# Performance work log

Hardware: AMD Instinct MI355X
Metric: run time of the kernel (lower is better)

The kernel has to match this reference:

```python
import jax, jax.numpy as jnp
import numpy as np

NUM_NODES = 2048   # N (spatial)
SEQ_LEN = 512      # T (temporal)
LATENT = 32
LAYERS = 2
SELF_LOOP_EPS = 0.5
B = 4


def setup_inputs() -> dict:
    key = jax.random.key(0)
    k1, k2, k3 = jax.random.split(key, 3)
    NT = NUM_NODES + SEQ_LEN
    X = jax.random.normal(k1, (B, NT, LATENT), dtype=jnp.float32)
    # GraphSAGE-style per-layer weights: self and neighbor transforms + bias
    Ws = jax.random.normal(k2, (LAYERS, LATENT, LATENT), dtype=jnp.float32) * 0.05
    Wn = jax.random.normal(k3, (LAYERS, LATENT, LATENT), dtype=jnp.float32) * 0.05
    b = jnp.zeros((LAYERS, LATENT), dtype=jnp.float32)
    return {"X": X, "Ws": Ws, "Wn": Wn, "b": b}


def build_adj(X):
    # node_embs = concat(spatial, temporal) == X itself
    adj = jnp.einsum('bnf,bmf->bnm', X, X)          # [B, N+T, N+T]
    adj = jnp.tanh(jax.nn.relu(adj))
    NT = X.shape[1]
    adj = adj + SELF_LOOP_EPS * jnp.eye(NT, dtype=adj.dtype)
    return adj


def reference(X, Ws, Wn, b):
    adj = build_adj(X)
    h = X
    # dense weighted aggregation == sparse message passing over nonzero edges,
    # since edge weights are exactly the adjacency values
    for l in range(LAYERS):
        agg = jnp.einsum('bnm,bmd->bnd', adj, h)    # neighbor aggregation
        h = jax.nn.elu(jnp.einsum('bnd,de->bne', h, Ws[l])
                       + jnp.einsum('bnd,de->bne', agg, Wn[l])
                       + b[l])
    return h
```

## Files before the change

### kernel.cpp

```cpp
#include <hip/hip_runtime.h>
#include <math.h>

#define NT 2560
#define DF 32
#define NB 4
#define SELF_EPS 0.5f
#define MS 8
#define MROWS (NT / MS)
#define MT 64
#define MITERS (MROWS / MT)
#define TN 64

typedef __attribute__((ext_vector_type(8))) short bf16x8;
typedef __attribute__((ext_vector_type(4))) float f32x4;

__device__ __forceinline__ unsigned short f2bf(float f) {
    unsigned u = __builtin_bit_cast(unsigned, f);
    u += 0x7fffu + ((u >> 16) & 1u);
    return (unsigned short)(u >> 16);
}

__device__ __forceinline__ float fast_rcp(float x) {
#if __has_builtin(__builtin_amdgcn_rcpf)
    return __builtin_amdgcn_rcpf(x);
#else
    return 1.0f / x;
#endif
}

__device__ __forceinline__ float fast_exp2(float x) {
#if __has_builtin(__builtin_amdgcn_exp2f)
    return __builtin_amdgcn_exp2f(x);
#else
    return exp2f(x);
#endif
}

__device__ __forceinline__ float tanh_relu(float x) {
    float m = fmaxf(x, 0.0f);
    float e = fast_exp2(m * 2.885390082f);
    return 1.0f - 2.0f * fast_rcp(e + 1.0f);
}

__global__ __launch_bounds__(256, 4)
void prep(const float* __restrict__ X,
          unsigned short* __restrict__ Xb, unsigned short* __restrict__ XT)
{
    const int t = threadIdx.x;
    __shared__ float sT[32][33];
    const int tile = blockIdx.x;
    const int b = tile / 80, n0 = (tile % 80) * 32;
    const int row = t >> 3, c4 = (t & 7) * 4;
    const size_t rbase = ((size_t)(b * NT + n0 + row)) * DF + c4;
    const float4 v = *(const float4*)(X + rbase);
    unsigned p0 = (unsigned)f2bf(v.x) | ((unsigned)f2bf(v.y) << 16);
    unsigned p1 = (unsigned)f2bf(v.z) | ((unsigned)f2bf(v.w) << 16);
    *(uint2*)(Xb + rbase) = make_uint2(p0, p1);
    sT[row][c4 + 0] = v.x; sT[row][c4 + 1] = v.y;
    sT[row][c4 + 2] = v.z; sT[row][c4 + 3] = v.w;
    __syncthreads();
    const int d = t >> 3, nq = (t & 7) * 4;
    unsigned q0 = (unsigned)f2bf(sT[nq + 0][d]) | ((unsigned)f2bf(sT[nq + 1][d]) << 16);
    unsigned q1 = (unsigned)f2bf(sT[nq + 2][d]) | ((unsigned)f2bf(sT[nq + 3][d]) << 16);
    *(uint2*)(XT + ((size_t)(b * DF + d)) * NT + n0 + nq) = make_uint2(q0, q1);
}

__global__ __launch_bounds__(256, 4)
void gsage_main(const unsigned short* __restrict__ Xb,
                const unsigned short* __restrict__ HT,
                float* __restrict__ part)
{
    __shared__ unsigned short XmL[64 * 40];
    __shared__ unsigned short HtL[32 * 72];
    __shared__ unsigned short Ss[4 * 16 * 72];

    const int t = threadIdx.x;
    const int w = t >> 6, lane = t & 63;
    const int q = lane >> 4, c = lane & 15;
    const int n0 = blockIdx.x * TN;
    const int slice = blockIdx.y;
    const int mbase = slice * MROWS;
    const int b = blockIdx.z;

    const size_t xbase = (size_t)b * NT * DF;
    const size_t tbase = (size_t)b * DF * NT;

    const bf16x8 bfn = *(const bf16x8*)(Xb + xbase + (size_t)(n0 + w * 16 + c) * DF + q * 8);

    f32x4 acc0 = {0.f, 0.f, 0.f, 0.f};
    f32x4 acc1 = {0.f, 0.f, 0.f, 0.f};

    const int xrow = t >> 2, xseg = t & 3;
    const int hrow = t >> 3, hseg = t & 7;

    uint4 xv = *(const uint4*)(Xb + xbase + (size_t)(mbase + xrow) * DF + xseg * 8);
    uint4 hv = *(const uint4*)(HT + tbase + (size_t)hrow * NT + mbase + hseg * 8);

    const int n_g = n0 + w * 16 + c;
    unsigned short* SsW = Ss + w * (16 * 72);

    for (int it = 0; it < MITERS; ++it) {
        const int m0 = mbase + it * MT;
        __syncthreads();
        *(uint4*)(XmL + xrow * 40 + xseg * 8) = xv;
        *(uint4*)(HtL + hrow * 72 + hseg * 8) = hv;
        if (it + 1 < MITERS) {
            const int m1 = m0 + MT;
            xv = *(const uint4*)(Xb + xbase + (size_t)(m1 + xrow) * DF + xseg * 8);
            hv = *(const uint4*)(HT + tbase + (size_t)hrow * NT + m1 + hseg * 8);
        }
        __syncthreads();

        #pragma unroll
        for (int t4 = 0; t4 < 4; ++t4) {
            const bf16x8 af = *(const bf16x8*)(XmL + (t4 * 16 + c) * 40 + q * 8);
            const f32x4 zero = {0.f, 0.f, 0.f, 0.f};
            f32x4 st = __builtin_amdgcn_mfma_f32_16x16x32_bf16(af, bfn, zero, 0, 0, 0);
            float v0 = tanh_relu(st[0]);
            float v1 = tanh_relu(st[1]);
            float v2 = tanh_relu(st[2]);
            float v3 = tanh_relu(st[3]);
            if ((n0 + w * 16 == m0 + t4 * 16) && (q == (c >> 2))) {
                const int r = c & 3;
                v0 += (r == 0) ? SELF_EPS : 0.f;
                v1 += (r == 1) ? SELF_EPS : 0.f;
                v2 += (r == 2) ? SELF_EPS : 0.f;
                v3 += (r == 3) ? SELF_EPS : 0.f;
            }
            unsigned p0 = (unsigned)f2bf(v0) | ((unsigned)f2bf(v1) << 16);
            unsigned p1 = (unsigned)f2bf(v2) | ((unsigned)f2bf(v3) << 16);
            *(uint2*)(SsW + c * 72 + t4 * 16 + q * 4) = make_uint2(p0, p1);
        }
        asm volatile("s_waitcnt lgkmcnt(0)" ::: "memory");

        #pragma unroll
        for (int kc = 0; kc < 2; ++kc) {
            const bf16x8 sf = *(const bf16x8*)(SsW + c * 72 + kc * 32 + q * 8);
            const bf16x8 h0 = *(const bf16x8*)(HtL + c * 72 + kc * 32 + q * 8);
            const bf16x8 h1 = *(const bf16x8*)(HtL + (16 + c) * 72 + kc * 32 + q * 8);
            acc0 = __builtin_amdgcn_mfma_f32_16x16x32_bf16(sf, h0, acc0, 0, 0, 0);
            acc1 = __builtin_amdgcn_mfma_f32_16x16x32_bf16(sf, h1, acc1, 0, 0, 0);
        }
    }

    float* pp = part + ((size_t)slice * NB) * NT * DF + xbase
                     + (size_t)(n0 + w * 16 + q * 4) * DF + c;
    #pragma unroll
    for (int r = 0; r < 4; ++r) {
        pp[(size_t)r * DF]      = acc0[r];
        pp[(size_t)r * DF + 16] = acc1[r];
    }
}

__global__ __launch_bounds__(256, 4)
void gsage_epi(const float* __restrict__ Hin, const float* __restrict__ part,
               const float* __restrict__ Wsl, const float* __restrict__ Wnl,
               const float* __restrict__ bl,
               float* __restrict__ Hout, unsigned short* __restrict__ HTout)
{
    __shared__ float sW[32][33], sN[32][33], sH[32][36], sA[32][36], sT[32][33];
    const int t = threadIdx.x;
    const int n0 = blockIdx.x * 32;
    const int b = blockIdx.y;
    const int row = t >> 3, c4 = (t & 7) * 4;
    const size_t rb = ((size_t)(b * NT + n0 + row)) * DF + c4;
    const float4 hv = *(const float4*)(Hin + rb);
    float4 av = make_float4(0.f, 0.f, 0.f, 0.f);
    #pragma unroll
    for (int s = 0; s < MS; ++s) {
        const float4 v = *(const float4*)(part + (size_t)s * NB * NT * DF + rb);
        av.x += v.x; av.y += v.y; av.z += v.z; av.w += v.w;
    }
    const float4 w0 = *(const float4*)(Wsl + row * DF + c4);
    const float4 w1 = *(const float4*)(Wnl + row * DF + c4);
    sH[row][c4+0]=hv.x; sH[row][c4+1]=hv.y; sH[row][c4+2]=hv.z; sH[row][c4+3]=hv.w;
    sA[row][c4+0]=av.x; sA[row][c4+1]=av.y; sA[row][c4+2]=av.z; sA[row][c4+3]=av.w;
    sW[row][c4+0]=w0.x; sW[row][c4+1]=w0.y; sW[row][c4+2]=w0.z; sW[row][c4+3]=w0.w;
    sN[row][c4+0]=w1.x; sN[row][c4+1]=w1.y; sN[row][c4+2]=w1.z; sN[row][c4+3]=w1.w;
    __syncthreads();

    float4 z = make_float4(bl[c4+0], bl[c4+1], bl[c4+2], bl[c4+3]);
    #pragma unroll
    for (int k = 0; k < DF; ++k) {
        const float hk = sH[row][k], ak = sA[row][k];
        z.x += hk * sW[k][c4+0] + ak * sN[k][c4+0];
        z.y += hk * sW[k][c4+1] + ak * sN[k][c4+1];
        z.z += hk * sW[k][c4+2] + ak * sN[k][c4+2];
        z.w += hk * sW[k][c4+3] + ak * sN[k][c4+3];
    }
    z.x = z.x > 0.f ? z.x : __expf(z.x) - 1.f;
    z.y = z.y > 0.f ? z.y : __expf(z.y) - 1.f;
    z.z = z.z > 0.f ? z.z : __expf(z.z) - 1.f;
    z.w = z.w > 0.f ? z.w : __expf(z.w) - 1.f;
    *(float4*)(Hout + rb) = z;

    if (HTout != nullptr) {
        sT[row][c4+0]=z.x; sT[row][c4+1]=z.y; sT[row][c4+2]=z.z; sT[row][c4+3]=z.w;
        __syncthreads();
        const int d = t >> 3, nq = (t & 7) * 4;
        unsigned q0 = (unsigned)f2bf(sT[nq+0][d]) | ((unsigned)f2bf(sT[nq+1][d]) << 16);
        unsigned q1 = (unsigned)f2bf(sT[nq+2][d]) | ((unsigned)f2bf(sT[nq+3][d]) << 16);
        *(uint2*)(HTout + ((size_t)(b * DF + d)) * NT + n0 + nq) = make_uint2(q0, q1);
    }
}

extern "C" void kernel_launch(void* const* d_in, const int* in_sizes, int n_in,
                              void* d_out, int out_size, void* d_ws, size_t ws_size,
                              hipStream_t stream) {
    const float* X  = (const float*)d_in[0];
    const float* Ws = (const float*)d_in[1];
    const float* Wn = (const float*)d_in[2];
    const float* bv = (const float*)d_in[3];
    float* out = (float*)d_out;

    char* ws = (char*)d_ws;
    float* part = (float*)ws;
    float* h1   = part + (size_t)MS * NB * NT * DF;
    unsigned short* Xb  = (unsigned short*)(ws + 11796480);
    unsigned short* XT  = Xb + (size_t)NB * NT * DF;
    unsigned short* H1T = XT + (size_t)NB * NT * DF;

    prep<<<320, 256, 0, stream>>>(X, Xb, XT);

    dim3 g(NT / TN, MS, NB);
    gsage_main<<<g, 256, 0, stream>>>(Xb, XT, part);
    gsage_epi<<<dim3(NT / 32, NB), 256, 0, stream>>>(X, part, Ws, Wn, bv, h1, H1T);
    gsage_main<<<g, 256, 0, stream>>>(Xb, H1T, part);
    gsage_epi<<<dim3(NT / 32, NB), 256, 0, stream>>>(h1, part, Ws + DF * DF, Wn + DF * DF,
                                                     bv + DF, out, nullptr);
}
```

Measured before the change: 106.1 us.

## Fuse prep and both layers into one cooperative kernel with grid sync

Replaces the five-launch pipeline (prep, two main passes with split-M partials, two epilogues) with a single cooperative kernel that uses grid.sync between stages. Each 128-thread block owns 16 output rows, and its two waves each cover half of the M range with per-wave LDS staging. The partial sums are reduced in shared memory and the epilogue runs in-block, which removes the partial-sum buffer traffic and the separate epilogue launches. The cost is far fewer rows per block, no cross-wave reuse of the X and H tiles, and grid-wide barriers, with a fallback to three separate launches if the cooperative launch fails.

Measured after the change: 409.3 us. +285.9%, slower.

```diff
diff --git a/kernel.cpp b/kernel.cpp
--- a/kernel.cpp
+++ b/kernel.cpp
@@ -1,15 +1,15 @@
 #include <hip/hip_runtime.h>
+#include <hip/hip_cooperative_groups.h>
 #include <math.h>
+
+namespace cg = cooperative_groups;
 
 #define NT 2560
 #define DF 32
 #define NB 4
 #define SELF_EPS 0.5f
-#define MS 8
-#define MROWS (NT / MS)
-#define MT 64
-#define MITERS (MROWS / MT)
-#define TN 64
+#define WREG 12032
+#define MITW 20
 
 typedef __attribute__((ext_vector_type(8))) short bf16x8;
 typedef __attribute__((ext_vector_type(4))) float f32x4;
@@ -19,7 +19,6 @@
     u += 0x7fffu + ((u >> 16) & 1u);
     return (unsigned short)(u >> 16);
 }
-
 __device__ __forceinline__ float fast_rcp(float x) {
 #if __has_builtin(__builtin_amdgcn_rcpf)
     return __builtin_amdgcn_rcpf(x);
@@ -27,7 +26,6 @@
     return 1.0f / x;
 #endif
 }
-
 __device__ __forceinline__ float fast_exp2(float x) {
 #if __has_builtin(__builtin_amdgcn_exp2f)
     return __builtin_amdgcn_exp2f(x);
@@ -35,92 +33,108 @@
     return exp2f(x);
 #endif
 }
-
 __device__ __forceinline__ float tanh_relu(float x) {
     float m = fmaxf(x, 0.0f);
     float e = fast_exp2(m * 2.885390082f);
     return 1.0f - 2.0f * fast_rcp(e + 1.0f);
 }
-
-__global__ __launch_bounds__(256, 4)
-void prep(const float* __restrict__ X,
-          unsigned short* __restrict__ Xb, unsigned short* __restrict__ XT)
-{
-    const int t = threadIdx.x;
-    __shared__ float sT[32][33];
-    const int tile = blockIdx.x;
-    const int b = tile / 80, n0 = (tile % 80) * 32;
+__device__ __forceinline__ float elu(float x) {
+    return x > 0.f ? x : fast_exp2(x * 1.442695041f) - 1.f;
+}
+
+
+__device__ __forceinline__ void prep_unit(const float* __restrict__ X,
+                                          unsigned short* __restrict__ Xb,
+                                          unsigned short* __restrict__ XT,
+                                          char* smem, int t, int blk)
+{
+    const int b = blk & 3, n0p = (blk >> 2) * 16;
+    float* sTp = (float*)smem;
     const int row = t >> 3, c4 = (t & 7) * 4;
-    const size_t rbase = ((size_t)(b * NT + n0 + row)) * DF + c4;
-    const float4 v = *(const float4*)(X + rbase);
+    const size_t off = ((size_t)b * NT + n0p + row) * DF + c4;
+    const float4 v = *(const float4*)(X + off);
     unsigned p0 = (unsigned)f2bf(v.x) | ((unsigned)f2bf(v.y) << 16);
     unsigned p1 = (unsigned)f2bf(v.z) | ((unsigned)f2bf(v.w) << 16);
-    *(uint2*)(Xb + rbase) = make_uint2(p0, p1);
-    sT[row][c4 + 0] = v.x; sT[row][c4 + 1] = v.y;
-    sT[row][c4 + 2] = v.z; sT[row][c4 + 3] = v.w;
+    *(uint2*)(Xb + off) = make_uint2(p0, p1);
+    sTp[row * 33 + c4 + 0] = v.x; sTp[row * 33 + c4 + 1] = v.y;
+    sTp[row * 33 + c4 + 2] = v.z; sTp[row * 33 + c4 + 3] = v.w;
     __syncthreads();
-    const int d = t >> 3, nq = (t & 7) * 4;
-    unsigned q0 = (unsigned)f2bf(sT[nq + 0][d]) | ((unsigned)f2bf(sT[nq + 1][d]) << 16);
-    unsigned q1 = (unsigned)f2bf(sT[nq + 2][d]) | ((unsigned)f2bf(sT[nq + 3][d]) << 16);
-    *(uint2*)(XT + ((size_t)(b * DF + d)) * NT + n0 + nq) = make_uint2(q0, q1);
-}
-
-__global__ __launch_bounds__(256, 4)
-void gsage_main(const unsigned short* __restrict__ Xb,
-                const unsigned short* __restrict__ HT,
-                float* __restrict__ part)
-{
-    __shared__ unsigned short XmL[64 * 40];
-    __shared__ unsigned short HtL[32 * 72];
-    __shared__ unsigned short Ss[4 * 16 * 72];
-
-    const int t = threadIdx.x;
+    const int d = t >> 2, mp = (t & 3) * 4;
+    unsigned q0 = (unsigned)f2bf(sTp[(mp + 0) * 33 + d])
+                | ((unsigned)f2bf(sTp[(mp + 1) * 33 + d]) << 16);
+    unsigned q1 = (unsigned)f2bf(sTp[(mp + 2) * 33 + d])
+                | ((unsigned)f2bf(sTp[(mp + 3) * 33 + d]) << 16);
+    *(uint2*)(XT + ((size_t)b * DF + d) * NT + n0p + mp) = make_uint2(q0, q1);
+}
+
+__device__ __forceinline__ void layer_pass(
+    const unsigned short* __restrict__ Xb,
+    const unsigned short* __restrict__ HT,
+    const float* __restrict__ Hin,
+    const float* __restrict__ Wsl, const float* __restrict__ Wnl,
+    const float* __restrict__ bl,
+    float* __restrict__ Hout,
+    unsigned short* __restrict__ HTout,
+    char* smem, int t, int blk)
+{
+    const int b  = blk & 3;
+    const int n0 = (blk >> 2) * 16;
     const int w = t >> 6, lane = t & 63;
     const int q = lane >> 4, c = lane & 15;
-    const int n0 = blockIdx.x * TN;
-    const int slice = blockIdx.y;
-    const int mbase = slice * MROWS;
-    const int b = blockIdx.z;
-
     const size_t xbase = (size_t)b * NT * DF;
     const size_t tbase = (size_t)b * DF * NT;
 
-    const bf16x8 bfn = *(const bf16x8*)(Xb + xbase + (size_t)(n0 + w * 16 + c) * DF + q * 8);
+    unsigned short* Sw = (unsigned short*)(smem + w * WREG);
+    unsigned short* Xw = (unsigned short*)(smem + w * WREG + 2304);
+    unsigned short* Hw = (unsigned short*)(smem + w * WREG + 7424);
+
+    const bf16x8 bfn = *(const bf16x8*)(Xb + xbase + (size_t)(n0 + c) * DF + q * 8);
 
     f32x4 acc0 = {0.f, 0.f, 0.f, 0.f};
     f32x4 acc1 = {0.f, 0.f, 0.f, 0.f};
-
-    const int xrow = t >> 2, xseg = t & 3;
-    const int hrow = t >> 3, hseg = t & 7;
-
-    uint4 xv = *(const uint4*)(Xb + xbase + (size_t)(mbase + xrow) * DF + xseg * 8);
-    uint4 hv = *(const uint4*)(HT + tbase + (size_t)hrow * NT + mbase + hseg * 8);
-
-    const int n_g = n0 + w * 16 + c;
-    unsigned short* SsW = Ss + w * (16 * 72);
-
-    for (int it = 0; it < MITERS; ++it) {
-        const int m0 = mbase + it * MT;
-        __syncthreads();
-        *(uint4*)(XmL + xrow * 40 + xseg * 8) = xv;
-        *(uint4*)(HtL + hrow * 72 + hseg * 8) = hv;
-        if (it + 1 < MITERS) {
-            const int m1 = m0 + MT;
-            xv = *(const uint4*)(Xb + xbase + (size_t)(m1 + xrow) * DF + xseg * 8);
-            hv = *(const uint4*)(HT + tbase + (size_t)hrow * NT + m1 + hseg * 8);
-        }
-        __syncthreads();
+    const int wbase = w * (NT / 2);
+    const int hd = lane & 31, hh = lane >> 5;
+
+    uint4 xv[4], hv[4];
+    {
+        const unsigned short* xs = Xb + xbase + (size_t)(wbase + lane) * DF;
+        const unsigned short* hs = HT + tbase + (size_t)hd * NT + wbase + hh * 32;
+        #pragma unroll
+        for (int k = 0; k < 4; ++k) {
+            xv[k] = *(const uint4*)(xs + k * 8);
+            hv[k] = *(const uint4*)(hs + k * 8);
+        }
+    }
+
+    for (int it = 0; it < MITW; ++it) {
+        const int m0 = wbase + it * 64;
+        #pragma unroll
+        for (int k = 0; k < 4; ++k) {
+            *(uint4*)(Xw + lane * 40 + k * 8) = xv[k];
+            *(uint4*)(Hw + hd * 72 + hh * 32 + k * 8) = hv[k];
+        }
+        if (it + 1 < MITW) {
+            const int m1 = m0 + 64;
+            const unsigned short* xs = Xb + xbase + (size_t)(m1 + lane) * DF;
+            const unsigned short* hs = HT + tbase + (size_t)hd * NT + m1 + hh * 32;
+            #pragma unroll
+            for (int k = 0; k < 4; ++k) {
+                xv[k] = *(const uint4*)(xs + k * 8);
+                hv[k] = *(const uint4*)(hs + k * 8);
+            }
+        }
+        asm volatile("s_waitcnt lgkmcnt(0)" ::: "memory");
 
         #pragma unroll
         for (int t4 = 0; t4 < 4; ++t4) {
-            const bf16x8 af = *(const bf16x8*)(XmL + (t4 * 16 + c) * 40 + q * 8);
+            const bf16x8 af = *(const bf16x8*)(Xw + (t4 * 16 + c) * 40 + q * 8);
             const f32x4 zero = {0.f, 0.f, 0.f, 0.f};
             f32x4 st = __builtin_amdgcn_mfma_f32_16x16x32_bf16(af, bfn, zero, 0, 0, 0);
             float v0 = tanh_relu(st[0]);
             float v1 = tanh_relu(st[1]);
             float v2 = tanh_relu(st[2]);
             float v3 = tanh_relu(st[3]);
-            if ((n0 + w * 16 == m0 + t4 * 16) && (q == (c >> 2))) {
+            if ((m0 + t4 * 16 == n0) && (q == (c >> 2))) {
                 const int r = c & 3;
                 v0 += (r == 0) ? SELF_EPS : 0.f;
                 v1 += (r == 1) ? SELF_EPS : 0.f;
@@ -129,79 +143,125 @@
             }
             unsigned p0 = (unsigned)f2bf(v0) | ((unsigned)f2bf(v1) << 16);
             unsigned p1 = (unsigned)f2bf(v2) | ((unsigned)f2bf(v3) << 16);
-            *(uint2*)(SsW + c * 72 + t4 * 16 + q * 4) = make_uint2(p0, p1);
+            *(uint2*)(Sw + c * 72 + t4 * 16 + q * 4) = make_uint2(p0, p1);
         }
         asm volatile("s_waitcnt lgkmcnt(0)" ::: "memory");
 
         #pragma unroll
         for (int kc = 0; kc < 2; ++kc) {
-            const bf16x8 sf = *(const bf16x8*)(SsW + c * 72 + kc * 32 + q * 8);
-            const bf16x8 h0 = *(const bf16x8*)(HtL + c * 72 + kc * 32 + q * 8);
-            const bf16x8 h1 = *(const bf16x8*)(HtL + (16 + c) * 72 + kc * 32 + q * 8);
+            const bf16x8 sf  = *(const bf16x8*)(Sw + c * 72 + kc * 32 + q * 8);
+            const bf16x8 h0  = *(const bf16x8*)(Hw + c * 72 + kc * 32 + q * 8);
+            const bf16x8 h1v = *(const bf16x8*)(Hw + (16 + c) * 72 + kc * 32 + q * 8);
             acc0 = __builtin_amdgcn_mfma_f32_16x16x32_bf16(sf, h0, acc0, 0, 0, 0);
-            acc1 = __builtin_amdgcn_mfma_f32_16x16x32_bf16(sf, h1, acc1, 0, 0, 0);
-        }
-    }
-
-    float* pp = part + ((size_t)slice * NB) * NT * DF + xbase
-                     + (size_t)(n0 + w * 16 + q * 4) * DF + c;
+            acc1 = __builtin_amdgcn_mfma_f32_16x16x32_bf16(sf, h1v, acc1, 0, 0, 0);
+        }
+    }
+
+    float* sF = (float*)(smem + w * WREG);
     #pragma unroll
     for (int r = 0; r < 4; ++r) {
-        pp[(size_t)r * DF]      = acc0[r];
-        pp[(size_t)r * DF + 16] = acc1[r];
-    }
-}
-
-__global__ __launch_bounds__(256, 4)
-void gsage_epi(const float* __restrict__ Hin, const float* __restrict__ part,
-               const float* __restrict__ Wsl, const float* __restrict__ Wnl,
-               const float* __restrict__ bl,
-               float* __restrict__ Hout, unsigned short* __restrict__ HTout)
-{
-    __shared__ float sW[32][33], sN[32][33], sH[32][36], sA[32][36], sT[32][33];
-    const int t = threadIdx.x;
-    const int n0 = blockIdx.x * 32;
-    const int b = blockIdx.y;
-    const int row = t >> 3, c4 = (t & 7) * 4;
-    const size_t rb = ((size_t)(b * NT + n0 + row)) * DF + c4;
-    const float4 hv = *(const float4*)(Hin + rb);
-    float4 av = make_float4(0.f, 0.f, 0.f, 0.f);
-    #pragma unroll
-    for (int s = 0; s < MS; ++s) {
-        const float4 v = *(const float4*)(part + (size_t)s * NB * NT * DF + rb);
-        av.x += v.x; av.y += v.y; av.z += v.z; av.w += v.w;
-    }
-    const float4 w0 = *(const float4*)(Wsl + row * DF + c4);
-    const float4 w1 = *(const float4*)(Wnl + row * DF + c4);
-    sH[row][c4+0]=hv.x; sH[row][c4+1]=hv.y; sH[row][c4+2]=hv.z; sH[row][c4+3]=hv.w;
-    sA[row][c4+0]=av.x; sA[row][c4+1]=av.y; sA[row][c4+2]=av.z; sA[row][c4+3]=av.w;
-    sW[row][c4+0]=w0.x; sW[row][c4+1]=w0.y; sW[row][c4+2]=w0.z; sW[row][c4+3]=w0.w;
-    sN[row][c4+0]=w1.x; sN[row][c4+1]=w1.y; sN[row][c4+2]=w1.z; sN[row][c4+3]=w1.w;
+        sF[(q * 4 + r) * 33 + c]      = acc0[r];
+        sF[(q * 4 + r) * 33 + c + 16] = acc1[r];
+    }
     __syncthreads();
 
-    float4 z = make_float4(bl[c4+0], bl[c4+1], bl[c4+2], bl[c4+3]);
+    float* sAgg = (float*)(smem + 2304);
+    float* sOut = (float*)(smem + 2304 + 2112);
+    float* sH   = (float*)(smem + 7424);
+    float* sW   = (float*)(smem + WREG + 2304);
+    float* sN   = (float*)(smem + WREG + 7424);
+
+    const int rn = t >> 3, c4 = (t & 7) * 4;
+    {
+        const float* f0 = (const float*)(smem);
+        const float* f1 = (const float*)(smem + WREG);
+        #pragma unroll
+        for (int j = 0; j < 4; ++j)
+            sAgg[rn * 33 + c4 + j] = f0[rn * 33 + c4 + j] + f1[rn * 33 + c4 + j];
+        const float4 hvv = *(const float4*)(Hin + ((size_t)b * NT + n0 + rn) * DF + c4);
+        sH[rn * 33 + c4 + 0] = hvv.x; sH[rn * 33 + c4 + 1] = hvv.y;
+        sH[rn * 33 + c4 + 2] = hvv.z; sH[rn * 33 + c4 + 3] = hvv.w;
+        #pragma unroll
+        for (int h = 0; h < 2; ++h) {
+            const int k = rn + h * 16;
+            const float4 w0 = *(const float4*)(Wsl + k * DF + c4);
+            const float4 w1 = *(const float4*)(Wnl + k * DF + c4);
+            sW[k * 33 + c4 + 0] = w0.x; sW[k * 33 + c4 + 1] = w0.y;
+            sW[k * 33 + c4 + 2] = w0.z; sW[k * 33 + c4 + 3] = w0.w;
+            sN[k * 33 + c4 + 0] = w1.x; sN[k * 33 + c4 + 1] = w1.y;
+            sN[k * 33 + c4 + 2] = w1.z; sN[k * 33 + c4 + 3] = w1.w;
+        }
+    }
+    __syncthreads();
+
+    float z0 = bl[c4 + 0], z1 = bl[c4 + 1], z2 = bl[c4 + 2], z3 = bl[c4 + 3];
     #pragma unroll
     for (int k = 0; k < DF; ++k) {
-        const float hk = sH[row][k], ak = sA[row][k];
-        z.x += hk * sW[k][c4+0] + ak * sN[k][c4+0];
-        z.y += hk * sW[k][c4+1] + ak * sN[k][c4+1];
-        z.z += hk * sW[k][c4+2] + ak * sN[k][c4+2];
-        z.w += hk * sW[k][c4+3] + ak * sN[k][c4+3];
-    }
-    z.x = z.x > 0.f ? z.x : __expf(z.x) - 1.f;
-    z.y = z.y > 0.f ? z.y : __expf(z.y) - 1.f;
-    z.z = z.z > 0.f ? z.z : __expf(z.z) - 1.f;
-    z.w = z.w > 0.f ? z.w : __expf(z.w) - 1.f;
-    *(float4*)(Hout + rb) = z;
+        const float hk = sH[rn * 33 + k], ak = sAgg[rn * 33 + k];
+        z0 += hk * sW[k * 33 + c4 + 0] + ak * sN[k * 33 + c4 + 0];
+        z1 += hk * sW[k * 33 + c4 + 1] + ak * sN[k * 33 + c4 + 1];
+        z2 += hk * sW[k * 33 + c4 + 2] + ak * sN[k * 33 + c4 + 2];
+        z3 += hk * sW[k * 33 + c4 + 3] + ak * sN[k * 33 + c4 + 3];
+    }
+    z0 = elu(z0); z1 = elu(z1); z2 = elu(z2); z3 = elu(z3);
+    *(float4*)(Hout + ((size_t)b * NT + n0 + rn) * DF + c4) =
+        make_float4(z0, z1, z2, z3);
 
     if (HTout != nullptr) {
-        sT[row][c4+0]=z.x; sT[row][c4+1]=z.y; sT[row][c4+2]=z.z; sT[row][c4+3]=z.w;
+        sOut[rn * 33 + c4 + 0] = z0; sOut[rn * 33 + c4 + 1] = z1;
+        sOut[rn * 33 + c4 + 2] = z2; sOut[rn * 33 + c4 + 3] = z3;
         __syncthreads();
-        const int d = t >> 3, nq = (t & 7) * 4;
-        unsigned q0 = (unsigned)f2bf(sT[nq+0][d]) | ((unsigned)f2bf(sT[nq+1][d]) << 16);
-        unsigned q1 = (unsigned)f2bf(sT[nq+2][d]) | ((unsigned)f2bf(sT[nq+3][d]) << 16);
-        *(uint2*)(HTout + ((size_t)(b * DF + d)) * NT + n0 + nq) = make_uint2(q0, q1);
-    }
+        const int d = t >> 2, mp = (t & 3) * 4;
+        unsigned q0 = (unsigned)f2bf(sOut[(mp + 0) * 33 + d])
+                    | ((unsigned)f2bf(sOut[(mp + 1) * 33 + d]) << 16);
+        unsigned q1 = (unsigned)f2bf(sOut[(mp + 2) * 33 + d])
+                    | ((unsigned)f2bf(sOut[(mp + 3) * 33 + d]) << 16);
+        *(uint2*)(HTout + ((size_t)b * DF + d) * NT + n0 + mp) = make_uint2(q0, q1);
+    }
+}
+
+__global__ __launch_bounds__(128, 2)
+void fused(const float* __restrict__ X, const float* __restrict__ Ws,
+           const float* __restrict__ Wn, const float* __restrict__ bv,
+           float* __restrict__ out, float* __restrict__ h1,
+           unsigned short* __restrict__ Xb, unsigned short* __restrict__ XT,
+           unsigned short* __restrict__ H1T)
+{
+    __shared__ __align__(16) char smem[2 * WREG];
+    cg::grid_group grid = cg::this_grid();
+    const int t = threadIdx.x, blk = blockIdx.x;
+
+    prep_unit(X, Xb, XT, smem, t, blk);
+    __threadfence();
+    grid.sync();
+
+    layer_pass(Xb, XT, X, Ws, Wn, bv, h1, H1T, smem, t, blk);
+    __threadfence();
+    grid.sync();
+
+    layer_pass(Xb, H1T, h1, Ws + DF * DF, Wn + DF * DF, bv + DF,
+               out, nullptr, smem, t, blk);
+}
+
+__global__ __launch_bounds__(128, 2)
+void k_prep(const float* __restrict__ X, unsigned short* __restrict__ Xb,
+            unsigned short* __restrict__ XT)
+{
+    __shared__ __align__(16) char smem[2 * WREG];
+    prep_unit(X, Xb, XT, smem, threadIdx.x, blockIdx.x);
+}
+
+__global__ __launch_bounds__(128, 2)
+void k_layer(const unsigned short* __restrict__ Xb,
+             const unsigned short* __restrict__ HT,
+             const float* __restrict__ Hin,
+             const float* __restrict__ Wsl, const float* __restrict__ Wnl,
+             const float* __restrict__ bl,
+             float* __restrict__ Hout, unsigned short* __restrict__ HTout)
+{
+    __shared__ __align__(16) char smem[2 * WREG];
+    layer_pass(Xb, HT, Hin, Wsl, Wnl, bl, Hout, HTout, smem,
+               threadIdx.x, blockIdx.x);
 }
 
 extern "C" void kernel_launch(void* const* d_in, const int* in_sizes, int n_in,
@@ -214,18 +274,24 @@
     float* out = (float*)d_out;
 
     char* ws = (char*)d_ws;
-    float* part = (float*)ws;
-    float* h1   = part + (size_t)MS * NB * NT * DF;
-    unsigned short* Xb  = (unsigned short*)(ws + 11796480);
+    float* h1 = (float*)ws;
+    unsigned short* Xb  = (unsigned short*)(ws + 1310720);
     unsigned short* XT  = Xb + (size_t)NB * NT * DF;
     unsigned short* H1T = XT + (size_t)NB * NT * DF;
 
-    prep<<<320, 256, 0, stream>>>(X, Xb, XT);
-
-    dim3 g(NT / TN, MS, NB);
-    gsage_main<<<g, 256, 0, stream>>>(Xb, XT, part);
-    gsage_epi<<<dim3(NT / 32, NB), 256, 0, stream>>>(X, part, Ws, Wn, bv, h1, H1T);
-    gsage_main<<<g, 256, 0, stream>>>(Xb, H1T, part);
-    gsage_epi<<<dim3(NT / 32, NB), 256, 0, stream>>>(h1, part, Ws + DF * DF, Wn + DF * DF,
-                                                     bv + DF, out, nullptr);
-}
+    const float* Ws1 = Ws + DF * DF;
+    const float* Wn1 = Wn + DF * DF;
+    const float* bv1 = bv + DF;
+
+    void* args[] = {(void*)&X, (void*)&Ws, (void*)&Wn, (void*)&bv,
+                    (void*)&out, (void*)&h1, (void*)&Xb, (void*)&XT, (void*)&H1T};
+    hipError_t err = hipLaunchCooperativeKernel((const void*)fused,
+                                                dim3(NB * (NT / 16)), dim3(128),
+                                                args, 0, stream);
+    if (err != hipSuccess) {
+        k_prep<<<dim3(NB * (NT / 16)), 128, 0, stream>>>(X, Xb, XT);
+        k_layer<<<dim3(NB * (NT / 16)), 128, 0, stream>>>(Xb, XT, X, Ws, Wn, bv, h1, H1T);
+        k_layer<<<dim3(NB * (NT / 16)), 128, 0, stream>>>(Xb, H1T, h1, Ws1, Wn1, bv1,
+                                                          out, nullptr);
+    }
+}
```

## Fuse aggregation and epilogue into one layer kernel with in-block split-K reduction

Applied to the files above, without the earlier changes.

Merges the aggregation kernel and the epilogue kernel into a single per-layer kernel. Each block now owns 16 output rows, and its four waves each cover a quarter of the M dimension using private LDS staging without block barriers. The partial sums are reduced in LDS before the weight transform and ELU. This removes the 8-slice global partial buffer and two kernel launches per layer. In exchange, each block repeats the 16-row tile work with less reuse of the staged X/H tiles and uses fewer resident blocks per CU.

After: 192.9 us. 1.82x slower.

```diff
diff --git a/kernel.cpp b/kernel.cpp
--- a/kernel.cpp
+++ b/kernel.cpp
@@ -5,11 +5,7 @@
 #define DF 32
 #define NB 4
 #define SELF_EPS 0.5f
-#define MS 8
-#define MROWS (NT / MS)
-#define MT 64
-#define MITERS (MROWS / MT)
-#define TN 64
+#define WREG 12800
 
 typedef __attribute__((ext_vector_type(8))) short bf16x8;
 typedef __attribute__((ext_vector_type(4))) float f32x4;
@@ -19,7 +15,6 @@
     u += 0x7fffu + ((u >> 16) & 1u);
     return (unsigned short)(u >> 16);
 }
-
 __device__ __forceinline__ float fast_rcp(float x) {
 #if __has_builtin(__builtin_amdgcn_rcpf)
     return __builtin_amdgcn_rcpf(x);
@@ -27,7 +22,6 @@
     return 1.0f / x;
 #endif
 }
-
 __device__ __forceinline__ float fast_exp2(float x) {
 #if __has_builtin(__builtin_amdgcn_exp2f)
     return __builtin_amdgcn_exp2f(x);
@@ -35,11 +29,13 @@
     return exp2f(x);
 #endif
 }
-
 __device__ __forceinline__ float tanh_relu(float x) {
     float m = fmaxf(x, 0.0f);
     float e = fast_exp2(m * 2.885390082f);
     return 1.0f - 2.0f * fast_rcp(e + 1.0f);
+}
+__device__ __forceinline__ float elu(float x) {
+    return x > 0.f ? x : fast_exp2(x * 1.442695041f) - 1.f;
 }
 
 __global__ __launch_bounds__(256, 4)
@@ -65,62 +61,78 @@
     *(uint2*)(XT + ((size_t)(b * DF + d)) * NT + n0 + nq) = make_uint2(q0, q1);
 }
 
-__global__ __launch_bounds__(256, 4)
-void gsage_main(const unsigned short* __restrict__ Xb,
-                const unsigned short* __restrict__ HT,
-                float* __restrict__ part)
+__global__ __launch_bounds__(256, 3)
+void k_layer(const unsigned short* __restrict__ Xb,
+             const unsigned short* __restrict__ HT,
+             const float* __restrict__ Hin,
+             const float* __restrict__ Wsl, const float* __restrict__ Wnl,
+             const float* __restrict__ bl,
+             float* __restrict__ Hout,
+             unsigned short* __restrict__ HTout)
 {
-    __shared__ unsigned short XmL[64 * 40];
-    __shared__ unsigned short HtL[32 * 72];
-    __shared__ unsigned short Ss[4 * 16 * 72];
-
-    const int t = threadIdx.x;
+    __shared__ __align__(16) char smem[4 * WREG];
+    const int t = threadIdx.x, blk = blockIdx.x;
+    const int g = blk & 7;
+    const int b = g & 3;
+    const int n0 = ((blk >> 3) + (g >> 2) * 80) * 16;
     const int w = t >> 6, lane = t & 63;
     const int q = lane >> 4, c = lane & 15;
-    const int n0 = blockIdx.x * TN;
-    const int slice = blockIdx.y;
-    const int mbase = slice * MROWS;
-    const int b = blockIdx.z;
-
     const size_t xbase = (size_t)b * NT * DF;
     const size_t tbase = (size_t)b * DF * NT;
 
-    const bf16x8 bfn = *(const bf16x8*)(Xb + xbase + (size_t)(n0 + w * 16 + c) * DF + q * 8);
+    unsigned short* Sw = (unsigned short*)(smem + w * WREG);
+    unsigned short* Xw = (unsigned short*)(smem + w * WREG + 2560);
+    unsigned short* Hw = (unsigned short*)(smem + w * WREG + 7680);
+
+    const bf16x8 bfn = *(const bf16x8*)(Xb + xbase + (size_t)(n0 + c) * DF + q * 8);
 
     f32x4 acc0 = {0.f, 0.f, 0.f, 0.f};
     f32x4 acc1 = {0.f, 0.f, 0.f, 0.f};
-
-    const int xrow = t >> 2, xseg = t & 3;
-    const int hrow = t >> 3, hseg = t & 7;
-
-    uint4 xv = *(const uint4*)(Xb + xbase + (size_t)(mbase + xrow) * DF + xseg * 8);
-    uint4 hv = *(const uint4*)(HT + tbase + (size_t)hrow * NT + mbase + hseg * 8);
-
-    const int n_g = n0 + w * 16 + c;
-    unsigned short* SsW = Ss + w * (16 * 72);
-
-    for (int it = 0; it < MITERS; ++it) {
-        const int m0 = mbase + it * MT;
-        __syncthreads();
-        *(uint4*)(XmL + xrow * 40 + xseg * 8) = xv;
-        *(uint4*)(HtL + hrow * 72 + hseg * 8) = hv;
-        if (it + 1 < MITERS) {
-            const int m1 = m0 + MT;
-            xv = *(const uint4*)(Xb + xbase + (size_t)(m1 + xrow) * DF + xseg * 8);
-            hv = *(const uint4*)(HT + tbase + (size_t)hrow * NT + m1 + hseg * 8);
-        }
-        __syncthreads();
+    const int wbase = w * (NT / 4);
+
+    const int xr = lane >> 2, xs = lane & 3;
+    const int hr = lane >> 3, hs = lane & 7;
+
+    uint4 xv[4], hv[4];
+    {
+        const unsigned short* xp = Xb + xbase + (size_t)wbase * DF;
+        const unsigned short* hp = HT + tbase + wbase;
+        #pragma unroll
+        for (int k = 0; k < 4; ++k) {
+            xv[k] = *(const uint4*)(xp + (size_t)(k * 16 + xr) * DF + xs * 8);
+            hv[k] = *(const uint4*)(hp + (size_t)(k * 8 + hr) * NT + hs * 8);
+        }
+    }
+
+    for (int it = 0; it < 10; ++it) {
+        const int m0 = wbase + it * 64;
+        #pragma unroll
+        for (int k = 0; k < 4; ++k) {
+            *(uint4*)(Xw + (k * 16 + xr) * 40 + xs * 8) = xv[k];
+            *(uint4*)(Hw + (k * 8 + hr) * 80 + hs * 8) = hv[k];
+        }
+        if (it + 1 < 10) {
+            const int m1 = m0 + 64;
+            const unsigned short* xp = Xb + xbase + (size_t)m1 * DF;
+            const unsigned short* hp = HT + tbase + m1;
+            #pragma unroll
+            for (int k = 0; k < 4; ++k) {
+                xv[k] = *(const uint4*)(xp + (size_t)(k * 16 + xr) * DF + xs * 8);
+                hv[k] = *(const uint4*)(hp + (size_t)(k * 8 + hr) * NT + hs * 8);
+            }
+        }
+        asm volatile("s_waitcnt lgkmcnt(0)" ::: "memory");
 
         #pragma unroll
         for (int t4 = 0; t4 < 4; ++t4) {
-            const bf16x8 af = *(const bf16x8*)(XmL + (t4 * 16 + c) * 40 + q * 8);
+            const bf16x8 af = *(const bf16x8*)(Xw + (t4 * 16 + c) * 40 + q * 8);
             const f32x4 zero = {0.f, 0.f, 0.f, 0.f};
             f32x4 st = __builtin_amdgcn_mfma_f32_16x16x32_bf16(af, bfn, zero, 0, 0, 0);
             float v0 = tanh_relu(st[0]);
             float v1 = tanh_relu(st[1]);
             float v2 = tanh_relu(st[2]);
             float v3 = tanh_relu(st[3]);
-            if ((n0 + w * 16 == m0 + t4 * 16) && (q == (c >> 2))) {
+            if ((m0 + t4 * 16 == n0) && (q == (c >> 2))) {
                 const int r = c & 3;
                 v0 += (r == 0) ? SELF_EPS : 0.f;
                 v1 += (r == 1) ? SELF_EPS : 0.f;
@@ -129,78 +141,78 @@
             }
             unsigned p0 = (unsigned)f2bf(v0) | ((unsigned)f2bf(v1) << 16);
             unsigned p1 = (unsigned)f2bf(v2) | ((unsigned)f2bf(v3) << 16);
-            *(uint2*)(SsW + c * 72 + t4 * 16 + q * 4) = make_uint2(p0, p1);
+            *(uint2*)(Sw + c * 80 + t4 * 16 + q * 4) = make_uint2(p0, p1);
         }
         asm volatile("s_waitcnt lgkmcnt(0)" ::: "memory");
 
         #pragma unroll
         for (int kc = 0; kc < 2; ++kc) {
-            const bf16x8 sf = *(const bf16x8*)(SsW + c * 72 + kc * 32 + q * 8);
-            const bf16x8 h0 = *(const bf16x8*)(HtL + c * 72 + kc * 32 + q * 8);
-            const bf16x8 h1 = *(const bf16x8*)(HtL + (16 + c) * 72 + kc * 32 + q * 8);
+            const bf16x8 sf  = *(const bf16x8*)(Sw + c * 80 + kc * 32 + q * 8);
+            const bf16x8 h0  = *(const bf16x8*)(Hw + c * 80 + kc * 32 + q * 8);
+            const bf16x8 h1v = *(const bf16x8*)(Hw + (16 + c) * 80 + kc * 32 + q * 8);
             acc0 = __builtin_amdgcn_mfma_f32_16x16x32_bf16(sf, h0, acc0, 0, 0, 0);
-            acc1 = __builtin_amdgcn_mfma_f32_16x16x32_bf16(sf, h1, acc1, 0, 0, 0);
-        }
-    }
-
-    float* pp = part + ((size_t)slice * NB) * NT * DF + xbase
-                     + (size_t)(n0 + w * 16 + q * 4) * DF + c;
+            acc1 = __builtin_amdgcn_mfma_f32_16x16x32_bf16(sf, h1v, acc1, 0, 0, 0);
+        }
+    }
+
+    float* sF = (float*)(smem + w * WREG);
     #pragma unroll
     for (int r = 0; r < 4; ++r) {
-        pp[(size_t)r * DF]      = acc0[r];
-        pp[(size_t)r * DF + 16] = acc1[r];
-    }
-}
-
-__global__ __launch_bounds__(256, 4)
-void gsage_epi(const float* __restrict__ Hin, const float* __restrict__ part,
-               const float* __restrict__ Wsl, const float* __restrict__ Wnl,
-               const float* __restrict__ bl,
-               float* __restrict__ Hout, unsigned short* __restrict__ HTout)
-{
-    __shared__ float sW[32][33], sN[32][33], sH[32][36], sA[32][36], sT[32][33];
-    const int t = threadIdx.x;
-    const int n0 = blockIdx.x * 32;
-    const int b = blockIdx.y;
-    const int row = t >> 3, c4 = (t & 7) * 4;
-    const size_t rb = ((size_t)(b * NT + n0 + row)) * DF + c4;
-    const float4 hv = *(const float4*)(Hin + rb);
-    float4 av = make_float4(0.f, 0.f, 0.f, 0.f);
-    #pragma unroll
-    for (int s = 0; s < MS; ++s) {
-        const float4 v = *(const float4*)(part + (size_t)s * NB * NT * DF + rb);
-        av.x += v.x; av.y += v.y; av.z += v.z; av.w += v.w;
-    }
-    const float4 w0 = *(const float4*)(Wsl + row * DF + c4);
-    const float4 w1 = *(const float4*)(Wnl + row * DF + c4);
-    sH[row][c4+0]=hv.x; sH[row][c4+1]=hv.y; sH[row][c4+2]=hv.z; sH[row][c4+3]=hv.w;
-    sA[row][c4+0]=av.x; sA[row][c4+1]=av.y; sA[row][c4+2]=av.z; sA[row][c4+3]=av.w;
-    sW[row][c4+0]=w0.x; sW[row][c4+1]=w0.y; sW[row][c4+2]=w0.z; sW[row][c4+3]=w0.w;
-    sN[row][c4+0]=w1.x; sN[row][c4+1]=w1.y; sN[row][c4+2]=w1.z; sN[row][c4+3]=w1.w;
+        sF[(q * 4 + r) * 33 + c]      = acc0[r];
+        sF[(q * 4 + r) * 33 + c + 16] = acc1[r];
+    }
     __syncthreads();
 
-    float4 z = make_float4(bl[c4+0], bl[c4+1], bl[c4+2], bl[c4+3]);
+    float* sAgg = (float*)(smem + 2560);
+    float* sH   = (float*)(smem + 7680);
+    float* sW   = (float*)(smem + WREG + 2560);
+    float* sN   = (float*)(smem + WREG + 7680);
+    float* sOut = (float*)(smem + 2 * WREG + 2560);
+
+    const int rn = t >> 4, dp = (t & 15) * 2;
+    {
+        float a0 = 0.f, a1 = 0.f;
+        #pragma unroll
+        for (int w2 = 0; w2 < 4; ++w2) {
+            const float* f = (const float*)(smem + w2 * WREG);
+            a0 += f[rn * 33 + dp];
+            a1 += f[rn * 33 + dp + 1];
+        }
+        sAgg[rn * 33 + dp]     = a0;
+        sAgg[rn * 33 + dp + 1] = a1;
+        const float2 hv2 = *(const float2*)(Hin + ((size_t)b * NT + n0 + rn) * DF + dp);
+        sH[rn * 33 + dp]     = hv2.x;
+        sH[rn * 33 + dp + 1] = hv2.y;
+    }
+    {
+        const int k = t >> 3, c4 = (t & 7) * 4;
+        const float4 w0 = *(const float4*)(Wsl + k * DF + c4);
+        const float4 w1 = *(const float4*)(Wnl + k * DF + c4);
+        sW[k * 33 + c4 + 0] = w0.x; sW[k * 33 + c4 + 1] = w0.y;
+        sW[k * 33 + c4 + 2] = w0.z; sW[k * 33 + c4 + 3] = w0.w;
+        sN[k * 33 + c4 + 0] = w1.x; sN[k * 33 + c4 + 1] = w1.y;
+        sN[k * 33 + c4 + 2] = w1.z; sN[k * 33 + c4 + 3] = w1.w;
+    }
+    __syncthreads();
+
+    float z0 = bl[dp], z1 = bl[dp + 1];
     #pragma unroll
     for (int k = 0; k < DF; ++k) {
-        const float hk = sH[row][k], ak = sA[row][k];
-        z.x += hk * sW[k][c4+0] + ak * sN[k][c4+0];
-        z.y += hk * sW[k][c4+1] + ak * sN[k][c4+1];
-        z.z += hk * sW[k][c4+2] + ak * sN[k][c4+2];
-        z.w += hk * sW[k][c4+3] + ak * sN[k][c4+3];
-    }
-    z.x = z.x > 0.f ? z.x : __expf(z.x) - 1.f;
-    z.y = z.y > 0.f ? z.y : __expf(z.y) - 1.f;
-    z.z = z.z > 0.f ? z.z : __expf(z.z) - 1.f;
-    z.w = z.w > 0.f ? z.w : __expf(z.w) - 1.f;
-    *(float4*)(Hout + rb) = z;
+        const float hk = sH[rn * 33 + k], ak = sAgg[rn * 33 + k];
+        z0 += hk * sW[k * 33 + dp]     + ak * sN[k * 33 + dp];
+        z1 += hk * sW[k * 33 + dp + 1] + ak * sN[k * 33 + dp + 1];
+    }
+    z0 = elu(z0); z1 = elu(z1);
+    *(float2*)(Hout + ((size_t)b * NT + n0 + rn) * DF + dp) = make_float2(z0, z1);
 
     if (HTout != nullptr) {
-        sT[row][c4+0]=z.x; sT[row][c4+1]=z.y; sT[row][c4+2]=z.z; sT[row][c4+3]=z.w;
+        sOut[rn * 33 + dp]     = z0;
+        sOut[rn * 33 + dp + 1] = z1;
         __syncthreads();
-        const int d = t >> 3, nq = (t & 7) * 4;
-        unsigned q0 = (unsigned)f2bf(sT[nq+0][d]) | ((unsigned)f2bf(sT[nq+1][d]) << 16);
-        unsigned q1 = (unsigned)f2bf(sT[nq+2][d]) | ((unsigned)f2bf(sT[nq+3][d]) << 16);
-        *(uint2*)(HTout + ((size_t)(b * DF + d)) * NT + n0 + nq) = make_uint2(q0, q1);
+        const int d = t >> 3, mp = (t & 7) * 2;
+        unsigned pv = (unsigned)f2bf(sOut[mp * 33 + d])
+                    | ((unsigned)f2bf(sOut[(mp + 1) * 33 + d]) << 16);
+        *(unsigned*)(HTout + ((size_t)b * DF + d) * NT + n0 + mp) = pv;
     }
 }
 
@@ -214,18 +226,13 @@
     float* out = (float*)d_out;
 
     char* ws = (char*)d_ws;
-    float* part = (float*)ws;
-    float* h1   = part + (size_t)MS * NB * NT * DF;
-    unsigned short* Xb  = (unsigned short*)(ws + 11796480);
+    float* h1 = (float*)ws;
+    unsigned short* Xb  = (unsigned short*)(ws + 1310720);
     unsigned short* XT  = Xb + (size_t)NB * NT * DF;
     unsigned short* H1T = XT + (size_t)NB * NT * DF;
 
     prep<<<320, 256, 0, stream>>>(X, Xb, XT);
-
-    dim3 g(NT / TN, MS, NB);
-    gsage_main<<<g, 256, 0, stream>>>(Xb, XT, part);
-    gsage_epi<<<dim3(NT / 32, NB), 256, 0, stream>>>(X, part, Ws, Wn, bv, h1, H1T);
-    gsage_main<<<g, 256, 0, stream>>>(Xb, H1T, part);
-    gsage_epi<<<dim3(NT / 32, NB), 256, 0, stream>>>(h1, part, Ws + DF * DF, Wn + DF * DF,
-                                                     bv + DF, out, nullptr);
-}
+    k_layer<<<640, 256, 0, stream>>>(Xb, XT, X, Ws, Wn, bv, h1, H1T);
+    k_layer<<<640, 256, 0, stream>>>(Xb, H1T, h1, Ws + DF * DF, Wn + DF * DF,
+                                     bv + DF, out, nullptr);
+}
```

## Fuse epilogue into main kernel via last-arriving-block atomic counter

Applied to the files above, without the earlier changes.

Folds the per-layer epilogue (partial-sum reduction, self/neighbor linear transforms, ELU, bf16 transpose) into the aggregation kernel. Each output tile counts finished slices with an atomic counter, and the last slice block does the reduction and epilogue. This removes two kernel launches and their inter-kernel gaps. It adds threadfences and atomics, leaves one block per tile doing a serial tail, and raises the launch bound to 5 blocks with a shared memory union.

Result: slower. 398.5 us (+275.7%).

```diff
diff --git a/kernel.cpp b/kernel.cpp
--- a/kernel.cpp
+++ b/kernel.cpp
@@ -19,7 +19,6 @@
     u += 0x7fffu + ((u >> 16) & 1u);
     return (unsigned short)(u >> 16);
 }
-
 __device__ __forceinline__ float fast_rcp(float x) {
 #if __has_builtin(__builtin_amdgcn_rcpf)
     return __builtin_amdgcn_rcpf(x);
@@ -27,7 +26,6 @@
     return 1.0f / x;
 #endif
 }
-
 __device__ __forceinline__ float fast_exp2(float x) {
 #if __has_builtin(__builtin_amdgcn_exp2f)
     return __builtin_amdgcn_exp2f(x);
@@ -35,18 +33,22 @@
     return exp2f(x);
 #endif
 }
-
 __device__ __forceinline__ float tanh_relu(float x) {
     float m = fmaxf(x, 0.0f);
     float e = fast_exp2(m * 2.885390082f);
     return 1.0f - 2.0f * fast_rcp(e + 1.0f);
 }
+__device__ __forceinline__ float elu(float x) {
+    return x > 0.f ? x : fast_exp2(x * 1.442695041f) - 1.f;
+}
 
 __global__ __launch_bounds__(256, 4)
 void prep(const float* __restrict__ X,
-          unsigned short* __restrict__ Xb, unsigned short* __restrict__ XT)
+          unsigned short* __restrict__ Xb, unsigned short* __restrict__ XT,
+          int* __restrict__ flags)
 {
     const int t = threadIdx.x;
+    if (t == 0) flags[blockIdx.x] = 0;
     __shared__ float sT[32][33];
     const int tile = blockIdx.x;
     const int b = tile / 80, n0 = (tile % 80) * 32;
@@ -65,14 +67,22 @@
     *(uint2*)(XT + ((size_t)(b * DF + d)) * NT + n0 + nq) = make_uint2(q0, q1);
 }
 
-__global__ __launch_bounds__(256, 4)
-void gsage_main(const unsigned short* __restrict__ Xb,
-                const unsigned short* __restrict__ HT,
-                float* __restrict__ part)
+__global__ __launch_bounds__(256, 5)
+void gsage_fused(const unsigned short* __restrict__ Xb,
+                 const unsigned short* __restrict__ HT,
+                 const float* __restrict__ Hin,
+                 const float* __restrict__ Wsl, const float* __restrict__ Wnl,
+                 const float* __restrict__ bl,
+                 float* __restrict__ part,
+                 int* __restrict__ flag,
+                 float* __restrict__ Hout,
+                 unsigned short* __restrict__ HTout)
 {
-    __shared__ unsigned short XmL[64 * 40];
-    __shared__ unsigned short HtL[32 * 72];
-    __shared__ unsigned short Ss[4 * 16 * 72];
+    __shared__ __align__(16) char smem[19200];
+    __shared__ int sLast;
+    unsigned short* Ss  = (unsigned short*)smem;
+    unsigned short* XmL = (unsigned short*)(smem + 9216);
+    unsigned short* HtL = (unsigned short*)(smem + 14336);
 
     const int t = threadIdx.x;
     const int w = t >> 6, lane = t & 63;
@@ -81,7 +91,6 @@
     const int slice = blockIdx.y;
     const int mbase = slice * MROWS;
     const int b = blockIdx.z;
-
     const size_t xbase = (size_t)b * NT * DF;
     const size_t tbase = (size_t)b * DF * NT;
 
@@ -96,8 +105,7 @@
     uint4 xv = *(const uint4*)(Xb + xbase + (size_t)(mbase + xrow) * DF + xseg * 8);
     uint4 hv = *(const uint4*)(HT + tbase + (size_t)hrow * NT + mbase + hseg * 8);
 
-    const int n_g = n0 + w * 16 + c;
-    unsigned short* SsW = Ss + w * (16 * 72);
+    unsigned short* SsW = Ss + w * 1152;
 
     for (int it = 0; it < MITERS; ++it) {
         const int m0 = mbase + it * MT;
@@ -135,11 +143,11 @@
 
         #pragma unroll
         for (int kc = 0; kc < 2; ++kc) {
-            const bf16x8 sf = *(const bf16x8*)(SsW + c * 72 + kc * 32 + q * 8);
-            const bf16x8 h0 = *(const bf16x8*)(HtL + c * 72 + kc * 32 + q * 8);
-            const bf16x8 h1 = *(const bf16x8*)(HtL + (16 + c) * 72 + kc * 32 + q * 8);
+            const bf16x8 sf  = *(const bf16x8*)(SsW + c * 72 + kc * 32 + q * 8);
+            const bf16x8 h0  = *(const bf16x8*)(HtL + c * 72 + kc * 32 + q * 8);
+            const bf16x8 h1v = *(const bf16x8*)(HtL + (16 + c) * 72 + kc * 32 + q * 8);
             acc0 = __builtin_amdgcn_mfma_f32_16x16x32_bf16(sf, h0, acc0, 0, 0, 0);
-            acc1 = __builtin_amdgcn_mfma_f32_16x16x32_bf16(sf, h1, acc1, 0, 0, 0);
+            acc1 = __builtin_amdgcn_mfma_f32_16x16x32_bf16(sf, h1v, acc1, 0, 0, 0);
         }
     }
 
@@ -150,57 +158,77 @@
         pp[(size_t)r * DF]      = acc0[r];
         pp[(size_t)r * DF + 16] = acc1[r];
     }
-}
-
-__global__ __launch_bounds__(256, 4)
-void gsage_epi(const float* __restrict__ Hin, const float* __restrict__ part,
-               const float* __restrict__ Wsl, const float* __restrict__ Wnl,
-               const float* __restrict__ bl,
-               float* __restrict__ Hout, unsigned short* __restrict__ HTout)
-{
-    __shared__ float sW[32][33], sN[32][33], sH[32][36], sA[32][36], sT[32][33];
-    const int t = threadIdx.x;
-    const int n0 = blockIdx.x * 32;
-    const int b = blockIdx.y;
-    const int row = t >> 3, c4 = (t & 7) * 4;
-    const size_t rb = ((size_t)(b * NT + n0 + row)) * DF + c4;
-    const float4 hv = *(const float4*)(Hin + rb);
-    float4 av = make_float4(0.f, 0.f, 0.f, 0.f);
-    #pragma unroll
-    for (int s = 0; s < MS; ++s) {
-        const float4 v = *(const float4*)(part + (size_t)s * NB * NT * DF + rb);
-        av.x += v.x; av.y += v.y; av.z += v.z; av.w += v.w;
-    }
-    const float4 w0 = *(const float4*)(Wsl + row * DF + c4);
-    const float4 w1 = *(const float4*)(Wnl + row * DF + c4);
-    sH[row][c4+0]=hv.x; sH[row][c4+1]=hv.y; sH[row][c4+2]=hv.z; sH[row][c4+3]=hv.w;
-    sA[row][c4+0]=av.x; sA[row][c4+1]=av.y; sA[row][c4+2]=av.z; sA[row][c4+3]=av.w;
-    sW[row][c4+0]=w0.x; sW[row][c4+1]=w0.y; sW[row][c4+2]=w0.z; sW[row][c4+3]=w0.w;
-    sN[row][c4+0]=w1.x; sN[row][c4+1]=w1.y; sN[row][c4+2]=w1.z; sN[row][c4+3]=w1.w;
+
+    __threadfence();
+    if (t == 0)
+        sLast = (atomicAdd(flag + blockIdx.z * 40 + blockIdx.x, 1) == MS - 1);
     __syncthreads();
-
-    float4 z = make_float4(bl[c4+0], bl[c4+1], bl[c4+2], bl[c4+3]);
+    if (!sLast) return;
+    __threadfence();
+
+    float* sAgg = (float*)smem;
+    float* sW   = (float*)(smem + 9216);
+    float* sN   = (float*)(smem + 14336);
+
+    const int row = t >> 2, ds0 = (t & 3) * 8;
+    {
+        float a[8];
+        #pragma unroll
+        for (int j = 0; j < 8; ++j) a[j] = 0.f;
+        #pragma unroll
+        for (int s = 0; s < MS; ++s) {
+            const float* p = part + ((size_t)s * NB + b) * NT * DF
+                                  + (size_t)(n0 + row) * DF + ds0;
+            const float4 u0 = *(const float4*)(p);
+            const float4 u1 = *(const float4*)(p + 4);
+            a[0] += u0.x; a[1] += u0.y; a[2] += u0.z; a[3] += u0.w;
+            a[4] += u1.x; a[5] += u1.y; a[6] += u1.z; a[7] += u1.w;
+        }
+        #pragma unroll
+        for (int j = 0; j < 8; ++j) sAgg[row * 33 + ds0 + j] = a[j];
+    }
+    {
+        const int k = t >> 3, c4 = (t & 7) * 4;
+        const float4 w0 = *(const float4*)(Wsl + k * DF + c4);
+        const float4 w1 = *(const float4*)(Wnl + k * DF + c4);
+        *(float4*)&sW[k * 36 + c4] = w0;
+        *(float4*)&sN[k * 36 + c4] = w1;
+    }
+    __syncthreads();
+
+    float z[8];
+    #pragma unroll
+    for (int j = 0; j < 8; ++j) z[j] = bl[ds0 + j];
+    const float* hrow2 = Hin + ((size_t)b * NT + n0 + row) * DF;
     #pragma unroll
     for (int k = 0; k < DF; ++k) {
-        const float hk = sH[row][k], ak = sA[row][k];
-        z.x += hk * sW[k][c4+0] + ak * sN[k][c4+0];
-        z.y += hk * sW[k][c4+1] + ak * sN[k][c4+1];
-        z.z += hk * sW[k][c4+2] + ak * sN[k][c4+2];
-        z.w += hk * sW[k][c4+3] + ak * sN[k][c4+3];
-    }
-    z.x = z.x > 0.f ? z.x : __expf(z.x) - 1.f;
-    z.y = z.y > 0.f ? z.y : __expf(z.y) - 1.f;
-    z.z = z.z > 0.f ? z.z : __expf(z.z) - 1.f;
-    z.w = z.w > 0.f ? z.w : __expf(z.w) - 1.f;
-    *(float4*)(Hout + rb) = z;
+        const float hk = hrow2[k];
+        const float ak = sAgg[row * 33 + k];
+        #pragma unroll
+        for (int j = 0; j < 8; ++j)
+            z[j] += hk * sW[k * 36 + ds0 + j] + ak * sN[k * 36 + ds0 + j];
+    }
+    #pragma unroll
+    for (int j = 0; j < 8; ++j) z[j] = elu(z[j]);
+    {
+        float* orow = Hout + ((size_t)b * NT + n0 + row) * DF + ds0;
+        *(float4*)orow       = make_float4(z[0], z[1], z[2], z[3]);
+        *(float4*)(orow + 4) = make_float4(z[4], z[5], z[6], z[7]);
+    }
 
     if (HTout != nullptr) {
-        sT[row][c4+0]=z.x; sT[row][c4+1]=z.y; sT[row][c4+2]=z.z; sT[row][c4+3]=z.w;
-        __syncthreads();
-        const int d = t >> 3, nq = (t & 7) * 4;
-        unsigned q0 = (unsigned)f2bf(sT[nq+0][d]) | ((unsigned)f2bf(sT[nq+1][d]) << 16);
-        unsigned q1 = (unsigned)f2bf(sT[nq+2][d]) | ((unsigned)f2bf(sT[nq+3][d]) << 16);
-        *(uint2*)(HTout + ((size_t)(b * DF + d)) * NT + n0 + nq) = make_uint2(q0, q1);
+        __syncthreads();
+        #pragma unroll
+        for (int j = 0; j < 8; ++j) sAgg[row * 33 + ds0 + j] = z[j];
+        __syncthreads();
+        const int d = t >> 3, mp = (t & 7) * 8;
+        unsigned pk[4];
+        #pragma unroll
+        for (int i = 0; i < 4; ++i)
+            pk[i] = (unsigned)f2bf(sAgg[(mp + 2 * i) * 33 + d])
+                  | ((unsigned)f2bf(sAgg[(mp + 2 * i + 1) * 33 + d]) << 16);
+        *(uint4*)(HTout + ((size_t)b * DF + d) * NT + n0 + mp) =
+            make_uint4(pk[0], pk[1], pk[2], pk[3]);
     }
 }
 
@@ -219,13 +247,13 @@
     unsigned short* Xb  = (unsigned short*)(ws + 11796480);
     unsigned short* XT  = Xb + (size_t)NB * NT * DF;
     unsigned short* H1T = XT + (size_t)NB * NT * DF;
-
-    prep<<<320, 256, 0, stream>>>(X, Xb, XT);
+    int* flags = (int*)(ws + 13762560);
+
+    prep<<<320, 256, 0, stream>>>(X, Xb, XT, flags);
 
     dim3 g(NT / TN, MS, NB);
-    gsage_main<<<g, 256, 0, stream>>>(Xb, XT, part);
-    gsage_epi<<<dim3(NT / 32, NB), 256, 0, stream>>>(X, part, Ws, Wn, bv, h1, H1T);
-    gsage_main<<<g, 256, 0, stream>>>(Xb, H1T, part);
-    gsage_epi<<<dim3(NT / 32, NB), 256, 0, stream>>>(h1, part, Ws + DF * DF, Wn + DF * DF,
-                                                     bv + DF, out, nullptr);
-}
+    gsage_fused<<<g, 256, 0, stream>>>(Xb, XT, X, Ws, Wn, bv,
+                                       part, flags, h1, H1T);
+    gsage_fused<<<g, 256, 0, stream>>>(Xb, H1T, h1, Ws + DF * DF, Wn + DF * DF,
+                                       bv + DF, part, flags + 160, out, nullptr);
+}
```
